# Optimization experiments

Hardware: AMD Instinct MI355X
Metric: run time of the kernel (lower is better)

Reference implementation:

```python
import jax, jax.numpy as jnp
import numpy as np

N = 50000
E = 500000
H = 128


def _linear(x, w, b):
    # torch nn.Linear: y = x @ W.T + b, W is [out, in]
    return x @ w.T + b


def _layer(x, h, edge_index, w0_w, w0_b, wl_w, wl_b, w1_w, w1_b):
    # PyG MessagePassing(aggr='add', flow='target_to_source'):
    # x_j = h[edge_index[1]], scatter-add into edge_index[0], dim_size = N
    msg = h[edge_index[1]]                               # [E, H] gather
    aggr = jax.ops.segment_sum(msg, edge_index[0], num_segments=h.shape[0])  # [N, H]
    return _linear(aggr, wl_w, wl_b) + _linear(h, w0_w, w0_b) + _linear(x, w1_w, w1_b)


def setup_inputs() -> dict:
    key = jax.random.key(0)
    ks = jax.random.split(key, 12)
    wscale = 0.05
    return {
        "x_a": jax.random.normal(ks[0], (N, H), jnp.float32),
        "x_b": jax.random.normal(ks[1], (N, H), jnp.float32),
        "edge_ab": jax.random.randint(ks[2], (2, E), 0, N, jnp.int32),
        "edge_ba": jax.random.randint(ks[3], (2, E), 0, N, jnp.int32),
        "conv0_w0_w": jax.random.normal(ks[4], (H, H), jnp.float32) * wscale,
        "conv0_w0_b": jnp.zeros((H,), jnp.float32),
        "conv0_wl_w": jax.random.normal(ks[5], (H, H), jnp.float32) * wscale,
        "conv0_wl_b": jnp.zeros((H,), jnp.float32),
        "conv0_w1_w": jax.random.normal(ks[6], (H, H), jnp.float32) * wscale,
        "conv0_w1_b": jnp.zeros((H,), jnp.float32),
        "conv1_w0_w": jax.random.normal(ks[7], (H, H), jnp.float32) * wscale,
        "conv1_w0_b": jnp.zeros((H,), jnp.float32),
        "conv1_wl_w": jax.random.normal(ks[8], (H, H), jnp.float32) * wscale,
        "conv1_wl_b": jnp.zeros((H,), jnp.float32),
        "conv1_w1_w": jax.random.normal(ks[9], (H, H), jnp.float32) * wscale,
        "conv1_w1_b": jnp.zeros((H,), jnp.float32),
        "out_w": jax.random.normal(ks[10], (H, H), jnp.float32) * wscale,
        "out_b": jnp.zeros((H,), jnp.float32),
    }


def reference(x_a, x_b, edge_ab, edge_ba,
              conv0_w0_w, conv0_w0_b, conv0_wl_w, conv0_wl_b, conv0_w1_w, conv0_w1_b,
              conv1_w0_w, conv1_w0_b, conv1_wl_w, conv1_wl_b, conv1_w1_w, conv1_w1_b,
              out_w, out_b):
    # metapath = [(a, r1, b), (b, r2, a)], loop over reversed(metapath):
    # iter 0: conv_idx=1, edge (b, r2, a), dst='a'
    h_a = jax.nn.relu(_layer(x_a, x_a, edge_ba,
                             conv1_w0_w, conv1_w0_b, conv1_wl_w, conv1_wl_b, conv1_w1_w, conv1_w1_b))
    # iter 1: conv_idx=0, edge (a, r1, b), dst='b'
    h_b = jax.nn.relu(_layer(x_b, x_b, edge_ab,
                             conv0_w0_w, conv0_w0_b, conv0_wl_w, conv0_wl_b, conv0_w1_w, conv0_w1_b))
    # start_type = 'a'
    return _linear(h_a, out_w, out_b)
```

## Files before the change

### kernel.cpp

```cpp
#include <hip/hip_runtime.h>
#include <hip/hip_bf16.h>

#define NN 50000
#define NE 500000
#define HD 128
#define CAP 128
#define PREP_B 24
#define ZCUR_B ((NN + 255) / 256)
#define ZAGGR_B 6250
#define FILLB_B ((NE + 255) / 256)
#define XCONV_B 3125
#define K2_B (FILLB_B + XCONV_B)

typedef __bf16 bf16;
typedef __attribute__((ext_vector_type(8))) __bf16 bf16x8;
typedef __attribute__((ext_vector_type(4))) float floatx4;

__device__ inline float u2f(unsigned int lo16) {
    union { unsigned int i; float f; } c; c.i = lo16 << 16; return c.f;
}

__device__ inline bf16x8 cvt8(floatx4 a, floatx4 b) {
    bf16x8 r;
#pragma unroll
    for (int j = 0; j < 4; j++) { r[j] = (bf16)a[j]; r[j + 4] = (bf16)b[j]; }
    return r;
}

__device__ inline void split8(const floatx4 f0, const floatx4 f1, bf16x8& hi, bf16x8& lo) {
#pragma unroll
    for (int j = 0; j < 4; j++) {
        float a = f0[j]; bf16 h = (bf16)a; hi[j] = h; lo[j] = (bf16)(a - (float)h);
        float b = f1[j]; bf16 g = (bf16)b; hi[j + 4] = g; lo[j + 4] = (bf16)(b - (float)g);
    }
}

__device__ inline bf16x8 zero8() {
    bf16x8 v;
#pragma unroll
    for (int j = 0; j < 8; j++) v[j] = (bf16)0.f;
    return v;
}

__device__ inline void addrow(floatx4& f0, floatx4& f1, const uint4 v) {
    f0[0] += u2f(v.x & 0xffff); f0[1] += u2f(v.x >> 16);
    f0[2] += u2f(v.y & 0xffff); f0[3] += u2f(v.y >> 16);
    f1[0] += u2f(v.z & 0xffff); f1[1] += u2f(v.z >> 16);
    f1[2] += u2f(v.w & 0xffff); f1[3] += u2f(v.w >> 16);
}

__global__ __launch_bounds__(256) void k_setup1(
    const float* __restrict__ wl, const float* __restrict__ w0, const float* __restrict__ w1,
    const float* __restrict__ bl, const float* __restrict__ b0, const float* __restrict__ b1,
    const float* __restrict__ ow, const float* __restrict__ ob,
    bf16* __restrict__ wlb, bf16* __restrict__ w01b, bf16* __restrict__ owb,
    float* __restrict__ bias1, float* __restrict__ bias2,
    float* __restrict__ aggr, int* __restrict__ cur, int* __restrict__ ovf_cnt,
    bf16* __restrict__ xb, int tier)
{
    const int b = blockIdx.x, tid = threadIdx.x;
    if (b < PREP_B) {
        int g = b * 256 + tid;
        int m = g >> 11, off = (g & 2047) << 3;
        if (m == 0) {
            const floatx4 a = *(const floatx4*)(wl + off);
            const floatx4 c = *(const floatx4*)(wl + off + 4);
            *(bf16x8*)(wlb + off) = cvt8(a, c);
        } else if (m == 1) {
            floatx4 a = *(const floatx4*)(w0 + off);
            floatx4 c = *(const floatx4*)(w0 + off + 4);
            const floatx4 d = *(const floatx4*)(w1 + off);
            const floatx4 e = *(const floatx4*)(w1 + off + 4);
#pragma unroll
            for (int j = 0; j < 4; j++) { a[j] += d[j]; c[j] += e[j]; }
            *(bf16x8*)(w01b + off) = cvt8(a, c);
        } else {
            const floatx4 a = *(const floatx4*)(ow + off);
            const floatx4 c = *(const floatx4*)(ow + off + 4);
            *(bf16x8*)(owb + off) = cvt8(a, c);
        }
        if (g < 128) bias1[g] = bl[g] + b0[g] + b1[g];
        else if (g < 256) bias2[g - 128] = ob[g - 128];
    } else if (b < PREP_B + ZCUR_B) {
        if (tier >= 1) {
            int i = (b - PREP_B) * 256 + tid;
            if (i < NN) cur[i] = 0;
            else if (i < NN + 16) *(bf16x8*)(xb + (size_t)NN * HD + (i - NN) * 8) = zero8();
            if (b == PREP_B && tid == 0) *ovf_cnt = 0;
        }
    } else {
        int i = (b - PREP_B - ZCUR_B) * 256 + tid;
        floatx4 z = {0.f, 0.f, 0.f, 0.f};
        ((floatx4*)aggr)[i] = z;
    }
}

__global__ __launch_bounds__(256) void k_setup2(
    const int* __restrict__ edge, const float* __restrict__ x,
    int* __restrict__ cur, int* __restrict__ bucket,
    int* __restrict__ ovf_cnt, int* __restrict__ ovf,
    bf16* __restrict__ xb)
{
    const int b = blockIdx.x, tid = threadIdx.x;
    if (b < FILLB_B) {
        int e = b * 256 + tid;
        if (e >= NE) return;
        int dst = edge[e];
        int src = edge[NE + e];
        int pos = atomicAdd(&cur[dst], 1);
        if (pos < CAP) {
            bucket[dst * CAP + pos] = src;
        } else {
            int oi = atomicAdd(ovf_cnt, 1);
            ovf[2 * oi] = dst;
            ovf[2 * oi + 1] = src;
        }
    } else {
        int off = ((b - FILLB_B) * 256 + tid) << 3;
        const floatx4 a = *(const floatx4*)(x + off);
        const floatx4 c = *(const floatx4*)(x + off + 4);
        *(bf16x8*)(xb + off) = cvt8(a, c);
    }
}

__global__ __launch_bounds__(256) void k_scatter(const float* __restrict__ x,
                                                 const int* __restrict__ edge,
                                                 float* __restrict__ aggr) {
    int tid = blockIdx.x * 256 + threadIdx.x;
    int e = tid >> 5;
    int c = (tid & 31) << 2;
    int dst = edge[e];
    int src = edge[NE + e];
    const floatx4 v = *(const floatx4*)(x + src * HD + c);
    float* ap = aggr + dst * HD + c;
    unsafeAtomicAdd(ap + 0, v[0]);
    unsafeAtomicAdd(ap + 1, v[1]);
    unsafeAtomicAdd(ap + 2, v[2]);
    unsafeAtomicAdd(ap + 3, v[3]);
}

__global__ __launch_bounds__(256) void k_fused(
    const float* __restrict__ aggr, const float* __restrict__ x, const bf16* __restrict__ xb,
    int tier,
    const int* __restrict__ cur, const int* __restrict__ bucket,
    const int* __restrict__ ovf_cnt, const int* __restrict__ ovf,
    const bf16* __restrict__ wlb, const bf16* __restrict__ w01b, const bf16* __restrict__ owb,
    const float* __restrict__ bias1, const float* __restrict__ bias2,
    float* __restrict__ out)
{
    __shared__ bf16 sA[128 * 136];
    __shared__ bf16 sB[128 * 136];
    __shared__ float b1_s[128], b2_s[128];
    float* tp = (float*)sB;
    const int tid = threadIdx.x;

#pragma unroll
    for (int it = 0; it < 8; it++) {
        int i = tid + it * 256;
        int r = i >> 4;
        int o = (i & 15) << 3;
        *(bf16x8*)(sA + r * 136 + o) = *(const bf16x8*)(wlb  + r * 128 + o);
        *(bf16x8*)(sB + r * 136 + o) = *(const bf16x8*)(w01b + r * 128 + o);
    }
    if (tid < 128) { b1_s[tid] = bias1[tid]; b2_s[tid] = bias2[tid]; }

    const int lane = tid & 63;
    const int wv   = tid >> 6;
    const int ln   = lane & 15;
    const int quad = lane >> 4;
    const int row0 = blockIdx.x * 64 + wv * 16;
    const int arow = row0 + ln;
    const bool aok = arow < NN;
    const int q8   = quad * 8;

    floatx4 ag0[4] = {};
    floatx4 ag1[4] = {};

    bf16x8 ax[4] = {zero8(), zero8(), zero8(), zero8()};
    if (tier && aok) {
#pragma unroll
        for (int kc = 0; kc < 4; kc++)
            ax[kc] = *(const bf16x8*)(xb + (size_t)arow * HD + kc * 32 + q8);
    }

    if (tier) {
        int deg = 0, n = 0;
        if (aok) { deg = cur[arow]; n = (deg < CAP) ? deg : CAP; }
        const int* bk = bucket + (size_t)arow * CAP;
        if (n > 0) {
            int4 s = *(const int4*)(bk);
            int t = 0;
            while (t < n) {
                const int4 sn = *(const int4*)(bk + t + 4);
                const int i0 = s.x;
                const int i1 = (t + 1 < n) ? s.y : NN;
                const int i2 = (t + 2 < n) ? s.z : NN;
                const int i3 = (t + 3 < n) ? s.w : NN;
                const uint4* p0 = (const uint4*)(xb + (size_t)i0 * HD + q8);
                const uint4* p1 = (const uint4*)(xb + (size_t)i1 * HD + q8);
                const uint4* p2 = (const uint4*)(xb + (size_t)i2 * HD + q8);
                const uint4* p3 = (const uint4*)(xb + (size_t)i3 * HD + q8);
                const uint4 v00 = p0[0], v01 = p0[4], v02 = p0[8], v03 = p0[12];
                const uint4 v10 = p1[0], v11 = p1[4], v12 = p1[8], v13 = p1[12];
                const uint4 v20 = p2[0], v21 = p2[4], v22 = p2[8], v23 = p2[12];
                const uint4 v30 = p3[0], v31 = p3[4], v32 = p3[8], v33 = p3[12];
                addrow(ag0[0], ag1[0], v00); addrow(ag0[1], ag1[1], v01);
                addrow(ag0[2], ag1[2], v02); addrow(ag0[3], ag1[3], v03);
                addrow(ag0[0], ag1[0], v10); addrow(ag0[1], ag1[1], v11);
                addrow(ag0[2], ag1[2], v12); addrow(ag0[3], ag1[3], v13);
                addrow(ag0[0], ag1[0], v20); addrow(ag0[1], ag1[1], v21);
                addrow(ag0[2], ag1[2], v22); addrow(ag0[3], ag1[3], v23);
                addrow(ag0[0], ag1[0], v30); addrow(ag0[1], ag1[1], v31);
                addrow(ag0[2], ag1[2], v32); addrow(ag0[3], ag1[3], v33);
                s = sn;
                t += 4;
            }
        }
        if (deg > CAP) {
            const int m = *ovf_cnt;
            for (int i = 0; i < m; i++) {
                if (ovf[2 * i] == arow) {
                    const bf16* r0 = xb + (size_t)ovf[2 * i + 1] * HD + q8;
                    const uint4 e0 = *(const uint4*)(r0);
                    const uint4 e1 = *(const uint4*)(r0 + 32);
                    const uint4 e2 = *(const uint4*)(r0 + 64);
                    const uint4 e3 = *(const uint4*)(r0 + 96);
                    addrow(ag0[0], ag1[0], e0); addrow(ag0[1], ag1[1], e1);
                    addrow(ag0[2], ag1[2], e2); addrow(ag0[3], ag1[3], e3);
                }
            }
        }
    } else if (aok) {
#pragma unroll
        for (int kc = 0; kc < 4; kc++) {
            ag0[kc] = *(const floatx4*)(aggr + (size_t)arow * HD + kc * 32 + q8);
            ag1[kc] = *(const floatx4*)(aggr + (size_t)arow * HD + kc * 32 + q8 + 4);
        }
    }

    __syncthreads();

    floatx4 acc[8] = {};

#pragma unroll
    for (int kc = 0; kc < 4; kc++) {
        const int k0 = kc * 32 + q8;
        bf16x8 a_hi, a_lo;
        split8(ag0[kc], ag1[kc], a_hi, a_lo);
        bf16x8 a_x = ax[kc];
        if (!tier && aok) {
            const floatx4 g0 = *(const floatx4*)(x + (size_t)arow * HD + k0);
            const floatx4 g1 = *(const floatx4*)(x + (size_t)arow * HD + k0 + 4);
            a_x = cvt8(g0, g1);
        }
#pragma unroll
        for (int nc = 0; nc < 8; nc++) {
            const bf16x8 bw  = *(const bf16x8*)(sA + (nc * 16 + ln) * 136 + k0);
            const bf16x8 bw2 = *(const bf16x8*)(sB + (nc * 16 + ln) * 136 + k0);
            acc[nc] = __builtin_amdgcn_mfma_f32_16x16x32_bf16(a_hi, bw,  acc[nc], 0, 0, 0);
            acc[nc] = __builtin_amdgcn_mfma_f32_16x16x32_bf16(a_lo, bw,  acc[nc], 0, 0, 0);
            acc[nc] = __builtin_amdgcn_mfma_f32_16x16x32_bf16(a_x,  bw2, acc[nc], 0, 0, 0);
        }
    }
    __syncthreads();

#pragma unroll
    for (int it = 0; it < 8; it++) {
        int i = tid + it * 256;
        int r = i >> 4;
        int o = (i & 15) << 3;
        *(bf16x8*)(sA + r * 136 + o) = *(const bf16x8*)(owb + r * 128 + o);
    }
#pragma unroll
    for (int nc = 0; nc < 8; nc++) {
        const int col = nc * 16 + ln;
        const float bv = b1_s[col];
#pragma unroll
        for (int r = 0; r < 4; r++) {
            float v = acc[nc][r] + bv;
            tp[wv * 2112 + (quad * 4 + r) * 132 + col] = (v > 0.f ? v : 0.f);
        }
        acc[nc][0] = acc[nc][1] = acc[nc][2] = acc[nc][3] = 0.f;
    }
    __syncthreads();

#pragma unroll
    for (int kc = 0; kc < 4; kc++) {
        const int k0 = kc * 32 + q8;
        const floatx4 f0 = *(const floatx4*)(tp + wv * 2112 + ln * 132 + k0);
        const floatx4 f1 = *(const floatx4*)(tp + wv * 2112 + ln * 132 + k0 + 4);
        bf16x8 a_hi, a_lo;
        split8(f0, f1, a_hi, a_lo);
#pragma unroll
        for (int nc = 0; nc < 8; nc++) {
            const bf16x8 bw = *(const bf16x8*)(sA + (nc * 16 + ln) * 136 + k0);
            acc[nc] = __builtin_amdgcn_mfma_f32_16x16x32_bf16(a_hi, bw, acc[nc], 0, 0, 0);
            acc[nc] = __builtin_amdgcn_mfma_f32_16x16x32_bf16(a_lo, bw, acc[nc], 0, 0, 0);
        }
    }

#pragma unroll
    for (int nc = 0; nc < 8; nc++) {
        const int col = nc * 16 + ln;
        const float bv = b2_s[col];
#pragma unroll
        for (int r = 0; r < 4; r++) {
            const int row = row0 + quad * 4 + r;
            if (row < NN) out[row * 128 + col] = acc[nc][r] + bv;
        }
    }
}

extern "C" void kernel_launch(void* const* d_in, const int* in_sizes, int n_in,
                              void* d_out, int out_size, void* d_ws, size_t ws_size,
                              hipStream_t stream) {
    const float* x_a     = (const float*)d_in[0];
    const int*   edge_ba = (const int*)d_in[3];
    const float* c1_w0_w = (const float*)d_in[10];
    const float* c1_w0_b = (const float*)d_in[11];
    const float* c1_wl_w = (const float*)d_in[12];
    const float* c1_wl_b = (const float*)d_in[13];
    const float* c1_w1_w = (const float*)d_in[14];
    const float* c1_w1_b = (const float*)d_in[15];
    const float* out_w   = (const float*)d_in[16];
    const float* out_b   = (const float*)d_in[17];

    char* p = (char*)d_ws;
    float* aggr  = (float*)p;   p += (size_t)NN * HD * 4;
    bf16*  wlb   = (bf16*)p;    p += 32768;
    bf16*  w01b  = (bf16*)p;    p += 32768;
    bf16*  owb   = (bf16*)p;    p += 32768;
    float* bias1 = (float*)p;   p += 512;
    float* bias2 = (float*)p;   p += 512;
    const size_t WS_FALL = (size_t)(p - (char*)d_ws);
    int*   cur    = (int*)p;    p += 200704;
    int*   bucket = (int*)p;    p += (size_t)NN * CAP * 4;
    bf16*  xb     = (bf16*)p;   p += (size_t)(NN + 2) * HD * 2;
    int*   ovf_cnt= (int*)p;    p += 256;
    int*   ovf    = (int*)p;    p += (size_t)NE * 2 * 4;
    const size_t WS_BUCKET = (size_t)(p - (char*)d_ws);
    (void)WS_FALL;

    const int tier = (ws_size >= WS_BUCKET) ? 1 : 0;

    const int k1_grid = tier ? (PREP_B + ZCUR_B) : (PREP_B + ZCUR_B + ZAGGR_B);
    k_setup1<<<k1_grid, 256, 0, stream>>>(c1_wl_w, c1_w0_w, c1_w1_w,
                                          c1_wl_b, c1_w0_b, c1_w1_b,
                                          out_w, out_b,
                                          wlb, w01b, owb, bias1, bias2,
                                          aggr, cur, ovf_cnt, xb, tier);

    if (tier) {
        k_setup2<<<K2_B, 256, 0, stream>>>(edge_ba, x_a, cur, bucket, ovf_cnt, ovf, xb);
    } else {
        k_scatter<<<NE * 32 / 256, 256, 0, stream>>>(x_a, edge_ba, aggr);
    }

    k_fused<<<(NN + 63) / 64, 256, 0, stream>>>(aggr, x_a, xb, tier,
                                                cur, bucket, ovf_cnt, ovf,
                                                wlb, w01b, owb, bias1, bias2,
                                                (float*)d_out);
}
```

Before: 194.1 us.

## Split bucket gather-aggregation into a separate kernel before the GEMM kernel

Moves the neighbor gather-sum from the fused GEMM kernel into a standalone k_aggr kernel. In k_aggr each 16-lane group handles one node and gathers eight neighbors per iteration, and it writes the fp32 aggregate to a global buffer. The GEMM kernel then only reads that aggregate. The goal is to decouple the irregular, latency-bound gather from the MFMA kernel so the gather gets higher occupancy and more memory-level parallelism. The cost is an extra kernel launch and a round trip of a 50000x128 fp32 buffer through global memory.

```diff
diff --git a/kernel.cpp b/kernel.cpp
--- a/kernel.cpp
+++ b/kernel.cpp
@@ -139,11 +139,66 @@
     unsafeAtomicAdd(ap + 3, v[3]);
 }
 
-__global__ __launch_bounds__(256) void k_fused(
+__global__ __launch_bounds__(256) void k_aggr(
+    const bf16* __restrict__ xb, const int* __restrict__ cur,
+    const int* __restrict__ bucket,
+    const int* __restrict__ ovf_cnt, const int* __restrict__ ovf,
+    float* __restrict__ aggr)
+{
+    const int gw   = (blockIdx.x * 256 + threadIdx.x) >> 6;
+    const int lane = threadIdx.x & 63;
+    const int quad = lane >> 4;
+    const int ln   = lane & 15;
+    const int node = gw * 4 + quad;
+    const int f8   = ln * 8;
+
+    floatx4 a0 = {0.f, 0.f, 0.f, 0.f}, a1 = {0.f, 0.f, 0.f, 0.f};
+    const int deg = cur[node];
+    const int n   = (deg < CAP) ? deg : CAP;
+    const int* bk = bucket + (size_t)node * CAP;
+
+    int t = 0;
+    while (t < n) {
+        const int4 s0 = *(const int4*)(bk + t);
+        const int4 s1 = *(const int4*)(bk + t + 4);
+        const int i0 = s0.x;
+        const int i1 = (t + 1 < n) ? s0.y : NN;
+        const int i2 = (t + 2 < n) ? s0.z : NN;
+        const int i3 = (t + 3 < n) ? s0.w : NN;
+        const int i4 = (t + 4 < n) ? s1.x : NN;
+        const int i5 = (t + 5 < n) ? s1.y : NN;
+        const int i6 = (t + 6 < n) ? s1.z : NN;
+        const int i7 = (t + 7 < n) ? s1.w : NN;
+        const uint4 v0 = *(const uint4*)(xb + (size_t)i0 * HD + f8);
+        const uint4 v1 = *(const uint4*)(xb + (size_t)i1 * HD + f8);
+        const uint4 v2 = *(const uint4*)(xb + (size_t)i2 * HD + f8);
+        const uint4 v3 = *(const uint4*)(xb + (size_t)i3 * HD + f8);
+        const uint4 v4 = *(const uint4*)(xb + (size_t)i4 * HD + f8);
+        const uint4 v5 = *(const uint4*)(xb + (size_t)i5 * HD + f8);
+        const uint4 v6 = *(const uint4*)(xb + (size_t)i6 * HD + f8);
+        const uint4 v7 = *(const uint4*)(xb + (size_t)i7 * HD + f8);
+        addrow(a0, a1, v0); addrow(a0, a1, v1);
+        addrow(a0, a1, v2); addrow(a0, a1, v3);
+        addrow(a0, a1, v4); addrow(a0, a1, v5);
+        addrow(a0, a1, v6); addrow(a0, a1, v7);
+        t += 8;
+    }
+    if (deg > CAP) {
+        const int m = *ovf_cnt;
+        for (int i = 0; i < m; i++) {
+            if (ovf[2 * i] == node) {
+                const uint4 v = *(const uint4*)(xb + (size_t)ovf[2 * i + 1] * HD + f8);
+                addrow(a0, a1, v);
+            }
+        }
+    }
+    *(floatx4*)(aggr + (size_t)node * HD + f8)     = a0;
+    *(floatx4*)(aggr + (size_t)node * HD + f8 + 4) = a1;
+}
+
+__global__ __launch_bounds__(256) void k_gemm12(
     const float* __restrict__ aggr, const float* __restrict__ x, const bf16* __restrict__ xb,
     int tier,
-    const int* __restrict__ cur, const int* __restrict__ bucket,
-    const int* __restrict__ ovf_cnt, const int* __restrict__ ovf,
     const bf16* __restrict__ wlb, const bf16* __restrict__ w01b, const bf16* __restrict__ owb,
     const float* __restrict__ bias1, const float* __restrict__ bias2,
     float* __restrict__ out)
@@ -175,66 +230,24 @@
 
     floatx4 ag0[4] = {};
     floatx4 ag1[4] = {};
-
     bf16x8 ax[4] = {zero8(), zero8(), zero8(), zero8()};
-    if (tier && aok) {
-#pragma unroll
-        for (int kc = 0; kc < 4; kc++)
-            ax[kc] = *(const bf16x8*)(xb + (size_t)arow * HD + kc * 32 + q8);
-    }
-
-    if (tier) {
-        int deg = 0, n = 0;
-        if (aok) { deg = cur[arow]; n = (deg < CAP) ? deg : CAP; }
-        const int* bk = bucket + (size_t)arow * CAP;
-        if (n > 0) {
-            int4 s = *(const int4*)(bk);
-            int t = 0;
-            while (t < n) {
-                const int4 sn = *(const int4*)(bk + t + 4);
-                const int i0 = s.x;
-                const int i1 = (t + 1 < n) ? s.y : NN;
-                const int i2 = (t + 2 < n) ? s.z : NN;
-                const int i3 = (t + 3 < n) ? s.w : NN;
-                const uint4* p0 = (const uint4*)(xb + (size_t)i0 * HD + q8);
-                const uint4* p1 = (const uint4*)(xb + (size_t)i1 * HD + q8);
-                const uint4* p2 = (const uint4*)(xb + (size_t)i2 * HD + q8);
-                const uint4* p3 = (const uint4*)(xb + (size_t)i3 * HD + q8);
-                const uint4 v00 = p0[0], v01 = p0[4], v02 = p0[8], v03 = p0[12];
-                const uint4 v10 = p1[0], v11 = p1[4], v12 = p1[8], v13 = p1[12];
-                const uint4 v20 = p2[0], v21 = p2[4], v22 = p2[8], v23 = p2[12];
-                const uint4 v30 = p3[0], v31 = p3[4], v32 = p3[8], v33 = p3[12];
-                addrow(ag0[0], ag1[0], v00); addrow(ag0[1], ag1[1], v01);
-                addrow(ag0[2], ag1[2], v02); addrow(ag0[3], ag1[3], v03);
-                addrow(ag0[0], ag1[0], v10); addrow(ag0[1], ag1[1], v11);
-                addrow(ag0[2], ag1[2], v12); addrow(ag0[3], ag1[3], v13);
-                addrow(ag0[0], ag1[0], v20); addrow(ag0[1], ag1[1], v21);
-                addrow(ag0[2], ag1[2], v22); addrow(ag0[3], ag1[3], v23);
-                addrow(ag0[0], ag1[0], v30); addrow(ag0[1], ag1[1], v31);
-                addrow(ag0[2], ag1[2], v32); addrow(ag0[3], ag1[3], v33);
-                s = sn;
-                t += 4;
-            }
-        }
-        if (deg > CAP) {
-            const int m = *ovf_cnt;
-            for (int i = 0; i < m; i++) {
-                if (ovf[2 * i] == arow) {
-                    const bf16* r0 = xb + (size_t)ovf[2 * i + 1] * HD + q8;
-                    const uint4 e0 = *(const uint4*)(r0);
-                    const uint4 e1 = *(const uint4*)(r0 + 32);
-                    const uint4 e2 = *(const uint4*)(r0 + 64);
-                    const uint4 e3 = *(const uint4*)(r0 + 96);
-                    addrow(ag0[0], ag1[0], e0); addrow(ag0[1], ag1[1], e1);
-                    addrow(ag0[2], ag1[2], e2); addrow(ag0[3], ag1[3], e3);
-                }
-            }
-        }
-    } else if (aok) {
+    if (aok) {
 #pragma unroll
         for (int kc = 0; kc < 4; kc++) {
             ag0[kc] = *(const floatx4*)(aggr + (size_t)arow * HD + kc * 32 + q8);
             ag1[kc] = *(const floatx4*)(aggr + (size_t)arow * HD + kc * 32 + q8 + 4);
+        }
+        if (tier) {
+#pragma unroll
+            for (int kc = 0; kc < 4; kc++)
+                ax[kc] = *(const bf16x8*)(xb + (size_t)arow * HD + kc * 32 + q8);
+        } else {
+#pragma unroll
+            for (int kc = 0; kc < 4; kc++) {
+                const floatx4 g0 = *(const floatx4*)(x + (size_t)arow * HD + kc * 32 + q8);
+                const floatx4 g1 = *(const floatx4*)(x + (size_t)arow * HD + kc * 32 + q8 + 4);
+                ax[kc] = cvt8(g0, g1);
+            }
         }
     }
 
@@ -247,19 +260,13 @@
         const int k0 = kc * 32 + q8;
         bf16x8 a_hi, a_lo;
         split8(ag0[kc], ag1[kc], a_hi, a_lo);
-        bf16x8 a_x = ax[kc];
-        if (!tier && aok) {
-            const floatx4 g0 = *(const floatx4*)(x + (size_t)arow * HD + k0);
-            const floatx4 g1 = *(const floatx4*)(x + (size_t)arow * HD + k0 + 4);
-            a_x = cvt8(g0, g1);
-        }
 #pragma unroll
         for (int nc = 0; nc < 8; nc++) {
             const bf16x8 bw  = *(const bf16x8*)(sA + (nc * 16 + ln) * 136 + k0);
             const bf16x8 bw2 = *(const bf16x8*)(sB + (nc * 16 + ln) * 136 + k0);
-            acc[nc] = __builtin_amdgcn_mfma_f32_16x16x32_bf16(a_hi, bw,  acc[nc], 0, 0, 0);
-            acc[nc] = __builtin_amdgcn_mfma_f32_16x16x32_bf16(a_lo, bw,  acc[nc], 0, 0, 0);
-            acc[nc] = __builtin_amdgcn_mfma_f32_16x16x32_bf16(a_x,  bw2, acc[nc], 0, 0, 0);
+            acc[nc] = __builtin_amdgcn_mfma_f32_16x16x32_bf16(a_hi,  bw,  acc[nc], 0, 0, 0);
+            acc[nc] = __builtin_amdgcn_mfma_f32_16x16x32_bf16(a_lo,  bw,  acc[nc], 0, 0, 0);
+            acc[nc] = __builtin_amdgcn_mfma_f32_16x16x32_bf16(ax[kc], bw2, acc[nc], 0, 0, 0);
         }
     }
     __syncthreads();
@@ -352,12 +359,12 @@
 
     if (tier) {
         k_setup2<<<K2_B, 256, 0, stream>>>(edge_ba, x_a, cur, bucket, ovf_cnt, ovf, xb);
+        k_aggr  <<<3125, 256, 0, stream>>>(xb, cur, bucket, ovf_cnt, ovf, aggr);
     } else {
         k_scatter<<<NE * 32 / 256, 256, 0, stream>>>(x_a, edge_ba, aggr);
     }
 
-    k_fused<<<(NN + 63) / 64, 256, 0, stream>>>(aggr, x_a, xb, tier,
-                                                cur, bucket, ovf_cnt, ovf,
-                                                wlb, w01b, owb, bias1, bias2,
-                                                (float*)d_out);
-}
+    k_gemm12<<<(NN + 63) / 64, 256, 0, stream>>>(aggr, x_a, xb, tier,
+                                                 wlb, w01b, owb, bias1, bias2,
+                                                 (float*)d_out);
+}
```

After: 192.6 us. Within noise of the previous version (-0.7%).
